# Optimization experiments

Measured on AMD Instinct MI355X. Metric: run time of the kernel, lower is better.

Reference implementation:

```python
import jax, jax.numpy as jnp
import numpy as np

B, N, C = 2, 200000, 16
D, H, W = 256, 256, 32
BOUNDS = ((-48.0, 48.0), (-48.0, 48.0), (-4.0, 1.5))


def setup_inputs() -> dict:
    key = jax.random.key(0)
    k1, k2 = jax.random.split(key)
    lo = jnp.array([b[0] for b in BOUNDS], dtype=jnp.float32)
    hi = jnp.array([b[1] for b in BOUNDS], dtype=jnp.float32)
    # points uniform in the coordinate bounds so they land in-grid
    u = jax.random.uniform(k1, (B, N, 3), dtype=jnp.float32)
    points = lo + u * (hi - lo)
    features = jax.random.normal(k2, (B, N, C), dtype=jnp.float32)
    return {"points": points, "features": features}


def _voxelize(pts, fts):
    # pts: [N,3], fts: [N,C] -> [C,D,H,W] mean-pooled voxel grid
    (x0, x1), (y0, y1), (z0, z1) = BOUNDS
    vx = jnp.clip(((pts[:, 0] - x0) / (x1 - x0) * D).astype(jnp.int32), 0, D - 1)
    vy = jnp.clip(((pts[:, 1] - y0) / (y1 - y0) * H).astype(jnp.int32), 0, H - 1)
    vz = jnp.clip(((pts[:, 2] - z0) / (z1 - z0) * W).astype(jnp.int32), 0, W - 1)
    flat = (vx * H + vy) * W + vz  # [N]
    V = D * H * W
    sums = jax.ops.segment_sum(fts, flat, num_segments=V)               # [V, C]
    counts = jax.ops.segment_sum(jnp.ones((pts.shape[0],), fts.dtype), flat, num_segments=V)  # [V]
    grid = jnp.where(counts[:, None] > 0, sums / jnp.maximum(counts[:, None], 1.0), 0.0)
    return grid.T.reshape(fts.shape[1], D, H, W)


def reference(points, features):
    return jax.vmap(_voxelize)(points, features)  # [B, C, D, H, W]
```

## Files before the change

kernel.cpp:

```cpp
#include <hip/hip_runtime.h>

namespace {

constexpr int B = 2;
constexpr int N = 200000;
constexpr int C = 16;
constexpr int D = 256;
constexpr int H = 256;
constexpr int W = 32;
constexpr int V = D * H * W;
constexpr int BV = B * V;
constexpr unsigned NIL = 0xFFFFFFFFu;

__device__ __forceinline__ int voxel_of(float x, float y, float z) {
    float fx = (x - (-48.0f)) / 96.0f * 256.0f;
    float fy = (y - (-48.0f)) / 96.0f * 256.0f;
    float fz = (z - (-4.0f)) / 5.5f * 32.0f;
    int vx = (int)fx;
    int vy = (int)fy;
    int vz = (int)fz;
    vx = vx < 0 ? 0 : (vx > D - 1 ? D - 1 : vx);
    vy = vy < 0 ? 0 : (vy > H - 1 ? H - 1 : vy);
    vz = vz < 0 ? 0 : (vz > W - 1 ? W - 1 : vz);
    return (vx * H + vy) * W + vz;
}


__global__ __launch_bounds__(256) void init_head(uint4* __restrict__ head4, int n4) {
    int i = blockIdx.x * blockDim.x + threadIdx.x;
    if (i < n4) head4[i] = make_uint4(NIL, NIL, NIL, NIL);
}

__global__ __launch_bounds__(256) void build_list(
    const float* __restrict__ pts, unsigned* __restrict__ head,
    unsigned* __restrict__ nxt) {
    int idx = blockIdx.x * blockDim.x + threadIdx.x;
    if (idx >= B * N) return;
    const float* p = pts + (size_t)idx * 3;
    int v = voxel_of(p[0], p[1], p[2]);
    int b = idx / N;
    unsigned old = atomicExch(head + (size_t)b * V + v, (unsigned)idx);
    nxt[idx] = old;
}

__global__ __launch_bounds__(256) void finalize(
    const unsigned* __restrict__ head, const unsigned* __restrict__ nxt,
    const float4* __restrict__ fts4, float* __restrict__ out) {
    int t = blockIdx.x * blockDim.x + threadIdx.x;
    if (t >= BV) return;
    int b = t >> 21;
    int v = t & (V - 1);

    unsigned h = head[t];

    float s[16];
#pragma unroll
    for (int c = 0; c < 16; ++c) s[c] = 0.f;
    float cnt = 0.f;
    unsigned nx = NIL;

    if (h != NIL) {
        const float4* fp = fts4 + (size_t)h * 4;
        float4 f0 = fp[0];
        float4 f1 = fp[1];
        float4 f2 = fp[2];
        float4 f3 = fp[3];
        nx = nxt[h];
        s[0]  = f0.x; s[1]  = f0.y; s[2]  = f0.z; s[3]  = f0.w;
        s[4]  = f1.x; s[5]  = f1.y; s[6]  = f1.z; s[7]  = f1.w;
        s[8]  = f2.x; s[9]  = f2.y; s[10] = f2.z; s[11] = f2.w;
        s[12] = f3.x; s[13] = f3.y; s[14] = f3.z; s[15] = f3.w;
        cnt = 1.f;
    }

    while (nx != NIL) {
        const float4* fp = fts4 + (size_t)nx * 4;
        float4 f0 = fp[0];
        float4 f1 = fp[1];
        float4 f2 = fp[2];
        float4 f3 = fp[3];
        unsigned nn = nxt[nx];
        s[0]  += f0.x; s[1]  += f0.y; s[2]  += f0.z; s[3]  += f0.w;
        s[4]  += f1.x; s[5]  += f1.y; s[6]  += f1.z; s[7]  += f1.w;
        s[8]  += f2.x; s[9]  += f2.y; s[10] += f2.z; s[11] += f2.w;
        s[12] += f3.x; s[13] += f3.y; s[14] += f3.z; s[15] += f3.w;
        cnt += 1.f;
        nx = nn;
    }

    if (cnt > 1.f) {
        float c = cnt;
#pragma unroll
        for (int k = 0; k < 16; ++k) s[k] /= c;
    }

    float* obase = out + (size_t)b * C * V + v;
#pragma unroll
    for (int c = 0; c < 16; ++c)
        obase[(size_t)c * V] = s[c];
}

__global__ __launch_bounds__(256) void zero_f4(float4* __restrict__ p, int n4) {
    int i = blockIdx.x * blockDim.x + threadIdx.x;
    if (i < n4) p[i] = make_float4(0.f, 0.f, 0.f, 0.f);
}

__global__ __launch_bounds__(256) void count_only(
    const float* __restrict__ pts, float* __restrict__ counts) {
    int idx = blockIdx.x * blockDim.x + threadIdx.x;
    if (idx >= B * N) return;
    int b = idx / N;
    const float* p = pts + (size_t)idx * 3;
    int v = voxel_of(p[0], p[1], p[2]);
    atomicAdd(counts + (size_t)b * V + v, 1.0f);
}

__global__ __launch_bounds__(256) void scatter_direct(
    const float* __restrict__ pts, const float* __restrict__ fts,
    const float* __restrict__ counts, float* __restrict__ out) {
    int idx = blockIdx.x * blockDim.x + threadIdx.x;
    if (idx >= B * N) return;
    int b = idx / N;
    const float* p = pts + (size_t)idx * 3;
    int v = voxel_of(p[0], p[1], p[2]);
    float cnt = counts[(size_t)b * V + v];
    const float* f = fts + (size_t)idx * C;
    float* o = out + (size_t)b * C * V + v;
#pragma unroll
    for (int c = 0; c < 16; ++c) atomicAdd(o + (size_t)c * V, f[c] / cnt);
}

}

extern "C" void kernel_launch(void* const* d_in, const int* in_sizes, int n_in,
                              void* d_out, int out_size, void* d_ws, size_t ws_size,
                              hipStream_t stream) {
    const float* pts = (const float*)d_in[0];
    const float* fts = (const float*)d_in[1];
    float* out = (float*)d_out;

    const int n_pts = B * N;
    const int pt_blocks = (n_pts + 255) / 256;

    const size_t head_bytes = (size_t)BV * sizeof(unsigned);
    const size_t nxt_bytes = (size_t)n_pts * sizeof(unsigned);

    if (ws_size >= head_bytes + nxt_bytes) {
        unsigned* head = (unsigned*)d_ws;
        unsigned* nxt = head + (size_t)BV;

        int head_n4 = BV / 4;
        init_head<<<(head_n4 + 255) / 256, 256, 0, stream>>>((uint4*)head, head_n4);
        build_list<<<pt_blocks, 256, 0, stream>>>(pts, head, nxt);

        int fin_threads = BV;
        finalize<<<(fin_threads + 255) / 256, 256, 0, stream>>>(
            head, nxt, (const float4*)fts, out);
    } else {
        float* counts = (float*)d_ws;
        int counts_f4 = BV / 4;
        zero_f4<<<(counts_f4 + 255) / 256, 256, 0, stream>>>((float4*)counts, counts_f4);
        int out_f4 = out_size / 4;
        zero_f4<<<(out_f4 + 255) / 256, 256, 0, stream>>>((float4*)out, out_f4);
        count_only<<<pt_blocks, 256, 0, stream>>>(pts, counts);
        scatter_direct<<<pt_blocks, 256, 0, stream>>>(pts, fts, counts, out);
    }
}
```

Before: 330.2 us.

## Fuse init, list build and gather into one cooperative persistent kernel

```diff
diff --git a/kernel.cpp b/kernel.cpp
--- a/kernel.cpp
+++ b/kernel.cpp
@@ -1,4 +1,7 @@
 #include <hip/hip_runtime.h>
+#include <hip/hip_cooperative_groups.h>
+
+namespace cg = cooperative_groups;
 
 namespace {
 
@@ -25,29 +28,9 @@
     return (vx * H + vy) * W + vz;
 }
 
-
-__global__ __launch_bounds__(256) void init_head(uint4* __restrict__ head4, int n4) {
-    int i = blockIdx.x * blockDim.x + threadIdx.x;
-    if (i < n4) head4[i] = make_uint4(NIL, NIL, NIL, NIL);
-}
-
-__global__ __launch_bounds__(256) void build_list(
-    const float* __restrict__ pts, unsigned* __restrict__ head,
-    unsigned* __restrict__ nxt) {
-    int idx = blockIdx.x * blockDim.x + threadIdx.x;
-    if (idx >= B * N) return;
-    const float* p = pts + (size_t)idx * 3;
-    int v = voxel_of(p[0], p[1], p[2]);
-    int b = idx / N;
-    unsigned old = atomicExch(head + (size_t)b * V + v, (unsigned)idx);
-    nxt[idx] = old;
-}
-
-__global__ __launch_bounds__(256) void finalize(
-    const unsigned* __restrict__ head, const unsigned* __restrict__ nxt,
+__device__ __forceinline__ void gather_one_voxel(
+    int t, const unsigned* __restrict__ head, const unsigned* __restrict__ nxt,
     const float4* __restrict__ fts4, float* __restrict__ out) {
-    int t = blockIdx.x * blockDim.x + threadIdx.x;
-    if (t >= BV) return;
     int b = t >> 21;
     int v = t & (V - 1);
 
@@ -100,6 +83,61 @@
         obase[(size_t)c * V] = s[c];
 }
 
+__global__ __launch_bounds__(256, 4) void fused_all(
+    const float* __restrict__ pts, const float4* __restrict__ fts4,
+    unsigned* __restrict__ head, unsigned* __restrict__ nxt,
+    float* __restrict__ out) {
+    cg::grid_group grid = cg::this_grid();
+    const int tid = blockIdx.x * blockDim.x + threadIdx.x;
+    const int nthr = gridDim.x * blockDim.x;
+
+    uint4* head4 = (uint4*)head;
+    for (int i = tid; i < BV / 4; i += nthr)
+        head4[i] = make_uint4(NIL, NIL, NIL, NIL);
+
+    __threadfence();
+    grid.sync();
+
+    for (int idx = tid; idx < B * N; idx += nthr) {
+        const float* p = pts + (size_t)idx * 3;
+        int v = voxel_of(p[0], p[1], p[2]);
+        int b = idx >= N ? 1 : 0;
+        unsigned old = atomicExch(head + (size_t)b * V + v, (unsigned)idx);
+        nxt[idx] = old;
+    }
+
+    __threadfence();
+    grid.sync();
+
+    for (int t = tid; t < BV; t += nthr)
+        gather_one_voxel(t, head, nxt, fts4, out);
+}
+
+__global__ __launch_bounds__(256) void init_head(uint4* __restrict__ head4, int n4) {
+    int i = blockIdx.x * blockDim.x + threadIdx.x;
+    if (i < n4) head4[i] = make_uint4(NIL, NIL, NIL, NIL);
+}
+
+__global__ __launch_bounds__(256) void build_list(
+    const float* __restrict__ pts, unsigned* __restrict__ head,
+    unsigned* __restrict__ nxt) {
+    int idx = blockIdx.x * blockDim.x + threadIdx.x;
+    if (idx >= B * N) return;
+    const float* p = pts + (size_t)idx * 3;
+    int v = voxel_of(p[0], p[1], p[2]);
+    int b = idx >= N ? 1 : 0;
+    unsigned old = atomicExch(head + (size_t)b * V + v, (unsigned)idx);
+    nxt[idx] = old;
+}
+
+__global__ __launch_bounds__(256) void finalize(
+    const unsigned* __restrict__ head, const unsigned* __restrict__ nxt,
+    const float4* __restrict__ fts4, float* __restrict__ out) {
+    int t = blockIdx.x * blockDim.x + threadIdx.x;
+    if (t >= BV) return;
+    gather_one_voxel(t, head, nxt, fts4, out);
+}
+
 __global__ __launch_bounds__(256) void zero_f4(float4* __restrict__ p, int n4) {
     int i = blockIdx.x * blockDim.x + threadIdx.x;
     if (i < n4) p[i] = make_float4(0.f, 0.f, 0.f, 0.f);
@@ -109,7 +147,7 @@
     const float* __restrict__ pts, float* __restrict__ counts) {
     int idx = blockIdx.x * blockDim.x + threadIdx.x;
     if (idx >= B * N) return;
-    int b = idx / N;
+    int b = idx >= N ? 1 : 0;
     const float* p = pts + (size_t)idx * 3;
     int v = voxel_of(p[0], p[1], p[2]);
     atomicAdd(counts + (size_t)b * V + v, 1.0f);
@@ -120,7 +158,7 @@
     const float* __restrict__ counts, float* __restrict__ out) {
     int idx = blockIdx.x * blockDim.x + threadIdx.x;
     if (idx >= B * N) return;
-    int b = idx / N;
+    int b = idx >= N ? 1 : 0;
     const float* p = pts + (size_t)idx * 3;
     int v = voxel_of(p[0], p[1], p[2]);
     float cnt = counts[(size_t)b * V + v];
@@ -149,13 +187,20 @@
         unsigned* head = (unsigned*)d_ws;
         unsigned* nxt = head + (size_t)BV;
 
-        int head_n4 = BV / 4;
-        init_head<<<(head_n4 + 255) / 256, 256, 0, stream>>>((uint4*)head, head_n4);
-        build_list<<<pt_blocks, 256, 0, stream>>>(pts, head, nxt);
-
-        int fin_threads = BV;
-        finalize<<<(fin_threads + 255) / 256, 256, 0, stream>>>(
-            head, nxt, (const float4*)fts, out);
+        const float4* fts4 = (const float4*)fts;
+        void* args[] = {(void*)&pts, (void*)&fts4, (void*)&head,
+                        (void*)&nxt, (void*)&out};
+        hipError_t e = hipLaunchCooperativeKernel(
+            (const void*)fused_all, dim3(1024), dim3(256), args, 0, stream);
+
+        if (e != hipSuccess) {
+            int head_n4 = BV / 4;
+            init_head<<<(head_n4 + 255) / 256, 256, 0, stream>>>(
+                (uint4*)head, head_n4);
+            build_list<<<pt_blocks, 256, 0, stream>>>(pts, head, nxt);
+            finalize<<<(BV + 255) / 256, 256, 0, stream>>>(
+                head, nxt, (const float4*)fts, out);
+        }
     } else {
         float* counts = (float*)d_ws;
         int counts_f4 = BV / 4;
```

Measured after the change: 668.3 us. 2.02x slower.

## Stage finalize outputs in shared memory tile and write float4 coalesced rows

Applied to the files above, without the earlier changes.

```diff
diff --git a/kernel.cpp b/kernel.cpp
--- a/kernel.cpp
+++ b/kernel.cpp
@@ -11,6 +11,7 @@
 constexpr int V = D * H * W;
 constexpr int BV = B * V;
 constexpr unsigned NIL = 0xFFFFFFFFu;
+constexpr int VOX = 512;
 
 __device__ __forceinline__ int voxel_of(float x, float y, float z) {
     float fx = (x - (-48.0f)) / 96.0f * 256.0f;
@@ -38,66 +39,88 @@
     if (idx >= B * N) return;
     const float* p = pts + (size_t)idx * 3;
     int v = voxel_of(p[0], p[1], p[2]);
-    int b = idx / N;
+    int b = idx >= N ? 1 : 0;
     unsigned old = atomicExch(head + (size_t)b * V + v, (unsigned)idx);
     nxt[idx] = old;
 }
 
-__global__ __launch_bounds__(256) void finalize(
+__global__ __launch_bounds__(256) void finalize_tile(
     const unsigned* __restrict__ head, const unsigned* __restrict__ nxt,
     const float4* __restrict__ fts4, float* __restrict__ out) {
-    int t = blockIdx.x * blockDim.x + threadIdx.x;
-    if (t >= BV) return;
-    int b = t >> 21;
-    int v = t & (V - 1);
+    __shared__ float tile[C][VOX];
 
-    unsigned h = head[t];
+    const int tid = threadIdx.x;
+    const int base = blockIdx.x * VOX;
+    const int b = base >> 21;
+    const int v0 = base & (V - 1);
 
-    float s[16];
+    unsigned h[2];
+    h[0] = head[base + tid];
+    h[1] = head[base + 256 + tid];
+
 #pragma unroll
-    for (int c = 0; c < 16; ++c) s[c] = 0.f;
-    float cnt = 0.f;
-    unsigned nx = NIL;
+    for (int k = 0; k < 2; ++k) {
+        float s[16];
+#pragma unroll
+        for (int c = 0; c < 16; ++c) s[c] = 0.f;
+        float cnt = 0.f;
+        unsigned nx = NIL;
 
-    if (h != NIL) {
-        const float4* fp = fts4 + (size_t)h * 4;
-        float4 f0 = fp[0];
-        float4 f1 = fp[1];
-        float4 f2 = fp[2];
-        float4 f3 = fp[3];
-        nx = nxt[h];
-        s[0]  = f0.x; s[1]  = f0.y; s[2]  = f0.z; s[3]  = f0.w;
-        s[4]  = f1.x; s[5]  = f1.y; s[6]  = f1.z; s[7]  = f1.w;
-        s[8]  = f2.x; s[9]  = f2.y; s[10] = f2.z; s[11] = f2.w;
-        s[12] = f3.x; s[13] = f3.y; s[14] = f3.z; s[15] = f3.w;
-        cnt = 1.f;
+        if (h[k] != NIL) {
+            const float4* fp = fts4 + (size_t)h[k] * 4;
+            float4 f0 = fp[0];
+            float4 f1 = fp[1];
+            float4 f2 = fp[2];
+            float4 f3 = fp[3];
+            nx = nxt[h[k]];
+            s[0]  = f0.x; s[1]  = f0.y; s[2]  = f0.z; s[3]  = f0.w;
+            s[4]  = f1.x; s[5]  = f1.y; s[6]  = f1.z; s[7]  = f1.w;
+            s[8]  = f2.x; s[9]  = f2.y; s[10] = f2.z; s[11] = f2.w;
+            s[12] = f3.x; s[13] = f3.y; s[14] = f3.z; s[15] = f3.w;
+            cnt = 1.f;
+        }
+
+        while (nx != NIL) {
+            const float4* fp = fts4 + (size_t)nx * 4;
+            float4 f0 = fp[0];
+            float4 f1 = fp[1];
+            float4 f2 = fp[2];
+            float4 f3 = fp[3];
+            unsigned nn = nxt[nx];
+            s[0]  += f0.x; s[1]  += f0.y; s[2]  += f0.z; s[3]  += f0.w;
+            s[4]  += f1.x; s[5]  += f1.y; s[6]  += f1.z; s[7]  += f1.w;
+            s[8]  += f2.x; s[9]  += f2.y; s[10] += f2.z; s[11] += f2.w;
+            s[12] += f3.x; s[13] += f3.y; s[14] += f3.z; s[15] += f3.w;
+            cnt += 1.f;
+            nx = nn;
+        }
+
+        if (cnt > 1.f) {
+            float c = cnt;
+#pragma unroll
+            for (int q = 0; q < 16; ++q) s[q] /= c;
+        }
+
+        int idx = k * 256 + tid;
+#pragma unroll
+        for (int c = 0; c < 16; ++c) tile[c][idx] = s[c];
     }
 
-    while (nx != NIL) {
-        const float4* fp = fts4 + (size_t)nx * 4;
-        float4 f0 = fp[0];
-        float4 f1 = fp[1];
-        float4 f2 = fp[2];
-        float4 f3 = fp[3];
-        unsigned nn = nxt[nx];
-        s[0]  += f0.x; s[1]  += f0.y; s[2]  += f0.z; s[3]  += f0.w;
-        s[4]  += f1.x; s[5]  += f1.y; s[6]  += f1.z; s[7]  += f1.w;
-        s[8]  += f2.x; s[9]  += f2.y; s[10] += f2.z; s[11] += f2.w;
-        s[12] += f3.x; s[13] += f3.y; s[14] += f3.z; s[15] += f3.w;
-        cnt += 1.f;
-        nx = nn;
+    __syncthreads();
+
+    const int w = tid >> 6;
+    const int l = tid & 63;
+    float* obase = out + (size_t)b * C * V + v0;
+#pragma unroll
+    for (int cc = 0; cc < 4; ++cc) {
+        int c = w * 4 + cc;
+#pragma unroll
+        for (int k = 0; k < VOX / 256; ++k) {
+            int idx = k * 64 + l;
+            float4 val = *(const float4*)&tile[c][idx * 4];
+            *(float4*)(obase + (size_t)c * V + idx * 4) = val;
+        }
     }
-
-    if (cnt > 1.f) {
-        float c = cnt;
-#pragma unroll
-        for (int k = 0; k < 16; ++k) s[k] /= c;
-    }
-
-    float* obase = out + (size_t)b * C * V + v;
-#pragma unroll
-    for (int c = 0; c < 16; ++c)
-        obase[(size_t)c * V] = s[c];
 }
 
 __global__ __launch_bounds__(256) void zero_f4(float4* __restrict__ p, int n4) {
@@ -109,7 +132,7 @@
     const float* __restrict__ pts, float* __restrict__ counts) {
     int idx = blockIdx.x * blockDim.x + threadIdx.x;
     if (idx >= B * N) return;
-    int b = idx / N;
+    int b = idx >= N ? 1 : 0;
     const float* p = pts + (size_t)idx * 3;
     int v = voxel_of(p[0], p[1], p[2]);
     atomicAdd(counts + (size_t)b * V + v, 1.0f);
@@ -120,7 +143,7 @@
     const float* __restrict__ counts, float* __restrict__ out) {
     int idx = blockIdx.x * blockDim.x + threadIdx.x;
     if (idx >= B * N) return;
-    int b = idx / N;
+    int b = idx >= N ? 1 : 0;
     const float* p = pts + (size_t)idx * 3;
     int v = voxel_of(p[0], p[1], p[2]);
     float cnt = counts[(size_t)b * V + v];
@@ -153,8 +176,8 @@
         init_head<<<(head_n4 + 255) / 256, 256, 0, stream>>>((uint4*)head, head_n4);
         build_list<<<pt_blocks, 256, 0, stream>>>(pts, head, nxt);
 
-        int fin_threads = BV;
-        finalize<<<(fin_threads + 255) / 256, 256, 0, stream>>>(
+        int fin_blocks = BV / VOX;
+        finalize_tile<<<fin_blocks, 256, 0, stream>>>(
             head, nxt, (const float4*)fts, out);
     } else {
         float* counts = (float*)d_ws;
```

Result: no change. 334.8 us (+1.4%).
